# Kernel tuning notes

Hardware: AMD Instinct MI355X
Metric: run time of the kernel (lower is better)

## Reference

```python
import jax, jax.numpy as jnp
import numpy as np

DIM = 512
NUM_HEADS = 16
HEAD_DIM = DIM // NUM_HEADS  # 32
SCALE = HEAD_DIM ** -0.5
B_, N = 1024, 49  # num_windows*batch, window_size**2


def setup_inputs() -> dict:
    key = jax.random.key(0)
    ks = jax.random.split(key, 12)
    s = DIM ** -0.5
    return {
        "x": jax.random.normal(ks[0], (B_, N, DIM), jnp.float32),
        "x2": jax.random.normal(ks[1], (B_, N, DIM), jnp.float32),
        "x3": jax.random.normal(ks[2], (B_, N, DIM), jnp.float32),
        # Linear weights stored as [in, out] (y = x @ W + b), same math as torch Linear
        "Wqkv": jax.random.normal(ks[3], (DIM, 3 * DIM), jnp.float32) * s,
        "bqkv": jnp.zeros((3 * DIM,), jnp.float32),
        "Wqkv2": jax.random.normal(ks[4], (DIM, 3 * DIM), jnp.float32) * s,
        "bqkv2": jnp.zeros((3 * DIM,), jnp.float32),
        "Wgw": jax.random.normal(ks[5], (DIM, DIM), jnp.float32) * s,
        "bgw": jnp.zeros((DIM,), jnp.float32),
        "Wproj": jax.random.normal(ks[6], (DIM, DIM), jnp.float32) * s,
        "bproj": jnp.zeros((DIM,), jnp.float32),
        "a": jnp.zeros((1,), jnp.float32),
    }


def reference(x, x2, x3, Wqkv, bqkv, Wqkv2, bqkv2, Wgw, bgw, Wproj, bproj, a):
    B, Nn, C = x.shape
    H, D = NUM_HEADS, HEAD_DIM
    # qkv from x: only k is actually used downstream
    qkv = (x @ Wqkv + bqkv).reshape(B, Nn, 3, H, D)
    k = jnp.transpose(qkv[:, :, 1], (0, 2, 1, 3))  # [B,H,N,D]
    # qkv2 from x3: q1 (gated query) and v1 (value + residual)
    qkv1 = (x3 @ Wqkv2 + bqkv2).reshape(B, Nn, 3, H, D)
    q1 = jnp.transpose(qkv1[:, :, 0], (0, 2, 1, 3))  # [B,H,N,D]
    v1 = jnp.transpose(qkv1[:, :, 2], (0, 2, 1, 3))  # [B,H,N,D]
    # gate from x2
    gw = jnp.transpose((x2 @ Wgw + bgw).reshape(B, Nn, H, D), (0, 2, 1, 3))
    q = q1 * SCALE * gw
    attn = jax.nn.softmax(jnp.einsum("bhnd,bhmd->bhnm", q, k), axis=-1)
    out = jnp.einsum("bhnm,bhmd->bhnd", attn, v1) + v1 * a
    out = jnp.transpose(out, (0, 2, 1, 3)).reshape(B, Nn, C)
    return out @ Wproj + bproj
```

## Files before the change

### kernel.cpp

```cpp
#include <hip/hip_runtime.h>

#define MR 50176
#define DIMC 512
#define NHEADS 16
#define NWIN 49
#define NBATCH 1024
#define ATTN_SCALE 0.17677669529663689f

typedef short bf16x8 __attribute__((ext_vector_type(8)));
typedef float f32x4 __attribute__((ext_vector_type(4)));
typedef unsigned int u32;

__device__ __forceinline__ unsigned short f2bf(float f) {
  union { float f; u32 u; } v; v.f = f;
  u32 u = v.u;
  u += 0x7FFFu + ((u >> 16) & 1u);
  return (unsigned short)(u >> 16);
}
__device__ __forceinline__ float bits_f(u32 u) {
  union { u32 u; float f; } v; v.u = u; return v.f;
}

__device__ __forceinline__ size_t pk_chunk(int r, int c) {
  return (((size_t)(r >> 3) * 8 + (c >> 3)) * 64 +
          ((r & 7) * 8 + ((c & 7) ^ (r & 7)))) << 4;
}

typedef const __attribute__((address_space(1))) u32* gp_t;
typedef __attribute__((address_space(3))) u32* lp_t;
__device__ __forceinline__ void glds16(const void* g, void* l) {
  __builtin_amdgcn_global_load_lds((gp_t)g, (lp_t)l, 16, 0, 0);
}

__global__ __launch_bounds__(256) void conv_pack(const float* __restrict__ X,
                                                 short* __restrict__ Xp) {
  const int tid = blockIdx.x * 256 + threadIdx.x;
  const int li = tid & 63, gl = tid >> 6;
  const int kline = gl & 7, group = gl >> 3;
  const int rr = li >> 3, pp = li & 7;
  const int row = group * 8 + rr;
  const int k = kline * 64 + ((pp ^ rr) << 3);
  const float* src = X + (size_t)row * DIMC + k;
  const float4 a = *(const float4*)src;
  const float4 b = *(const float4*)(src + 4);
  u32 w0 = (u32)f2bf(a.x) | ((u32)f2bf(a.y) << 16);
  u32 w1 = (u32)f2bf(a.z) | ((u32)f2bf(a.w) << 16);
  u32 w2 = (u32)f2bf(b.x) | ((u32)f2bf(b.y) << 16);
  u32 w3 = (u32)f2bf(b.z) | ((u32)f2bf(b.w) << 16);
  ((uint4*)Xp)[tid] = make_uint4(w0, w1, w2, w3);
}

__global__ __launch_bounds__(256) void prep_w_pack(
    const float* __restrict__ Wqkv, const float* __restrict__ Wqkv2,
    const float* __restrict__ Wgw, const float* __restrict__ Wproj,
    short* __restrict__ Wp) {
  const int tid = blockIdx.x * 256 + threadIdx.x;
  const int li = tid & 63, gl = tid >> 6;
  const int kline = gl & 7, group = gl >> 3;
  const int rr = li >> 3, pp = li & 7;
  const int row = group * 8 + rr;
  const int k = kline * 64 + ((pp ^ rr) << 3);
  const int n = row & 511, mat = row >> 9;
  const float* W; int ldw, col;
  if (mat == 0)      { W = Wqkv;  ldw = 1536; col = 512 + n; }
  else if (mat == 1) { W = Wqkv2; ldw = 1536; col = n; }
  else if (mat == 2) { W = Wqkv2; ldw = 1536; col = 1024 + n; }
  else if (mat == 3) { W = Wgw;   ldw = 512;  col = n; }
  else               { W = Wproj; ldw = 512;  col = n; }
  unsigned short h[8];
#pragma unroll
  for (int j = 0; j < 8; ++j) h[j] = f2bf(W[(size_t)(k + j) * ldw + col]);
  u32 w0 = (u32)h[0] | ((u32)h[1] << 16);
  u32 w1 = (u32)h[2] | ((u32)h[3] << 16);
  u32 w2 = (u32)h[4] | ((u32)h[5] << 16);
  u32 w3 = (u32)h[6] | ((u32)h[7] << 16);
  ((uint4*)Wp)[tid] = make_uint4(w0, w1, w2, w3);
}

template <bool OUT_F32>
__global__ __launch_bounds__(256) void gemm_glds(
    const short* __restrict__ Ap, const short* __restrict__ Wp, int wrow0,
    const float* __restrict__ bias0, const float* __restrict__ bias1,
    short* __restrict__ out0, short* __restrict__ out1,
    float* __restrict__ outf, int nsplit) {
  __shared__ short As[128 * 64];
  __shared__ short Bs[128 * 64];

  const int t = threadIdx.x, w = t >> 6, lane = t & 63;
  const int l15 = lane & 15, q = lane >> 4;
  const int wm = w >> 1, wn = w & 1;
  const int bx = blockIdx.x;
  const int row0 = blockIdx.y * 128;
  const int nw0 = wrow0 + bx * 128;
  const int colsel = (bx < nsplit) ? bx : bx - nsplit;
  const float* bias = (bx < nsplit) ? bias0 : bias1;
  short* outb = (bx < nsplit) ? out0 : out1;
  const int col0 = colsel * 128;

  f32x4 acc[4][4];
#pragma unroll
  for (int i = 0; i < 4; ++i)
#pragma unroll
    for (int j = 0; j < 4; ++j) acc[i][j] = {0.f, 0.f, 0.f, 0.f};

  const size_t lb = (size_t)lane * 16;
  const int r7 = l15 & 7, hi8 = l15 >> 3;

  for (int kt = 0; kt < 8; ++kt) {
    __syncthreads();
#pragma unroll
    for (int jj = 0; jj < 4; ++jj) {
      const int rg = w * 4 + jj;
      const char* ga = (const char*)Ap + ((((size_t)(row0 >> 3) + rg) * 8 + kt) << 10);
      glds16(ga + lb, &As[(size_t)rg << 9]);
      const char* gb = (const char*)Wp + ((((size_t)(nw0 >> 3) + rg) * 8 + kt) << 10);
      glds16(gb + lb, &Bs[(size_t)rg << 9]);
    }
    __syncthreads();
#pragma unroll
    for (int s = 0; s < 2; ++s) {
      const int sw = ((s * 4 + q) ^ r7);
      const int pos = (r7 * 8 + sw) * 8;
      bf16x8 af[4], bfr[4];
#pragma unroll
      for (int i = 0; i < 4; ++i)
        af[i] = *(const bf16x8*)&As[((wm * 8 + i * 2 + hi8) << 9) + pos];
#pragma unroll
      for (int j = 0; j < 4; ++j)
        bfr[j] = *(const bf16x8*)&Bs[((wn * 8 + j * 2 + hi8) << 9) + pos];
#pragma unroll
      for (int i = 0; i < 4; ++i)
#pragma unroll
        for (int j = 0; j < 4; ++j)
          acc[i][j] = __builtin_amdgcn_mfma_f32_16x16x32_bf16(af[i], bfr[j],
                                                              acc[i][j], 0, 0, 0);
    }
  }

#pragma unroll
  for (int j = 0; j < 4; ++j) {
    const int C = col0 + wn * 64 + j * 16 + l15;
    const float bv = bias[C];
#pragma unroll
    for (int i = 0; i < 4; ++i) {
#pragma unroll
      for (int r = 0; r < 4; ++r) {
        const int R = row0 + wm * 64 + i * 16 + q * 4 + r;
        const float val = acc[i][j][r] + bv;
        if constexpr (OUT_F32)
          outf[(size_t)R * DIMC + C] = val;
        else
          *(short*)((char*)outb + pk_chunk(R, C >> 3) + ((C & 7) << 1)) =
              (short)f2bf(val);
      }
    }
  }
}

__global__ __launch_bounds__(256) void attn_mfma(
    const short* __restrict__ kbuf, const short* __restrict__ qbuf,
    const short* __restrict__ vbuf, const short* __restrict__ gbuf,
    const float* __restrict__ a_scalar, short* __restrict__ obuf) {
  __shared__ short pls[4][64 * 40];
  __shared__ short vls[4][32 * 72];

  const int t = threadIdx.x;
  const int w = t >> 6, lane = t & 63;
  const int l15 = lane & 15, q = lane >> 4;
  const int wid = blockIdx.x * 4 + w;
  const int b = wid >> 4, h = wid & 15;
  const int row0 = b * NWIN;
  const float aval = a_scalar[0];
  short* P = pls[w];
  short* VT = vls[w];

#pragma unroll
  for (int it = 0; it < 5; ++it) {
    int off = (it * 64 + lane) * 8;
    if (off < 32 * 72) *(uint4*)&VT[off] = make_uint4(0u, 0u, 0u, 0u);
  }

  bf16x8 kf[4];
#pragma unroll
  for (int mj = 0; mj < 4; ++mj) {
    int m = mj * 16 + l15; if (m > 48) m = 48;
    kf[mj] = *(const bf16x8*)((const char*)kbuf + pk_chunk(row0 + m, h * 4 + q));
  }
  bf16x8 qf[4];
#pragma unroll
  for (int mi = 0; mi < 4; ++mi) {
    int n = mi * 16 + l15; if (n > 48) n = 48;
    const size_t off = pk_chunk(row0 + n, h * 4 + q);
    uint4 qa = *(const uint4*)((const char*)qbuf + off);
    uint4 ga = *(const uint4*)((const char*)gbuf + off);
    u32* qa_ = (u32*)&qa;
    u32* ga_ = (u32*)&ga;
    uint4 res; u32* r_ = (u32*)&res;
#pragma unroll
    for (int jj = 0; jj < 4; ++jj) {
      float lo = bits_f(qa_[jj] << 16) * bits_f(ga_[jj] << 16);
      float hi = bits_f(qa_[jj] & 0xffff0000u) * bits_f(ga_[jj] & 0xffff0000u);
      r_[jj] = (u32)f2bf(lo) | ((u32)f2bf(hi) << 16);
    }
    qf[mi] = *(bf16x8*)&res;
  }
#pragma unroll
  for (int it = 0; it < 4; ++it) {
    int chunk = it * 64 + lane;
    if (chunk < 196) {
      int n = chunk >> 2, dcq = chunk & 3;
      uint4 v = *(const uint4*)((const char*)vbuf + pk_chunk(row0 + n, h * 4 + dcq));
      const short* vs = (const short*)&v;
#pragma unroll
      for (int j = 0; j < 8; ++j) VT[(dcq * 8 + j) * 72 + n] = vs[j];
    }
  }

  f32x4 s[4][4];
#pragma unroll
  for (int mi = 0; mi < 4; ++mi)
#pragma unroll
    for (int nj = 0; nj < 4; ++nj) {
      f32x4 z = {0.f, 0.f, 0.f, 0.f};
      s[mi][nj] = __builtin_amdgcn_mfma_f32_16x16x32_bf16(qf[mi], kf[nj], z, 0, 0, 0);
    }

#pragma unroll
  for (int mi = 0; mi < 4; ++mi)
#pragma unroll
    for (int nj = 0; nj < 4; ++nj) {
      const bool valid = (nj * 16 + l15) < NWIN;
#pragma unroll
      for (int r = 0; r < 4; ++r)
        s[mi][nj][r] = valid ? __expf(ATTN_SCALE * s[mi][nj][r]) : 0.f;
    }

  float lsum[4][4];
#pragma unroll
  for (int mi = 0; mi < 4; ++mi)
#pragma unroll
    for (int r = 0; r < 4; ++r) {
      float part = s[mi][0][r] + s[mi][1][r] + s[mi][2][r] + s[mi][3][r];
      part += __shfl_xor(part, 1, 64);
      part += __shfl_xor(part, 2, 64);
      part += __shfl_xor(part, 4, 64);
      part += __shfl_xor(part, 8, 64);
      lsum[mi][r] = part;
    }

  f32x4 o[4][2];
#pragma unroll
  for (int mi = 0; mi < 4; ++mi)
#pragma unroll
    for (int dj = 0; dj < 2; ++dj) o[mi][dj] = {0.f, 0.f, 0.f, 0.f};

#pragma unroll
  for (int c = 0; c < 2; ++c) {
#pragma unroll
    for (int mi = 0; mi < 4; ++mi)
#pragma unroll
      for (int njh = 0; njh < 2; ++njh) {
        const int nj = c * 2 + njh;
        const int m = nj * 16 + l15;
#pragma unroll
        for (int r = 0; r < 4; ++r) {
          const int n = mi * 16 + q * 4 + r;
          float val = s[mi][nj][r];
          if (m == n) val += aval * lsum[mi][r];
          P[n * 40 + njh * 16 + l15] = (short)f2bf(val);
        }
      }
    bf16x8 bfr[2];
#pragma unroll
    for (int dj = 0; dj < 2; ++dj)
      bfr[dj] = *(const bf16x8*)&VT[(dj * 16 + l15) * 72 + c * 32 + q * 8];
#pragma unroll
    for (int mi = 0; mi < 4; ++mi) {
      bf16x8 af = *(const bf16x8*)&P[(mi * 16 + l15) * 40 + q * 8];
#pragma unroll
      for (int dj = 0; dj < 2; ++dj)
        o[mi][dj] = __builtin_amdgcn_mfma_f32_16x16x32_bf16(af, bfr[dj],
                                                            o[mi][dj], 0, 0, 0);
    }
  }

#pragma unroll
  for (int mi = 0; mi < 4; ++mi)
#pragma unroll
    for (int r = 0; r < 4; ++r) {
      const int n = mi * 16 + q * 4 + r;
      if (n < NWIN) {
        const float rl = 1.0f / lsum[mi][r];
#pragma unroll
        for (int dj = 0; dj < 2; ++dj) {
          const int d = dj * 16 + l15;
          *(short*)((char*)obuf + pk_chunk(row0 + n, h * 4 + (d >> 3)) +
                    ((d & 7) << 1)) = (short)f2bf(o[mi][dj][r] * rl);
        }
      }
    }
}

extern "C" void kernel_launch(void* const* d_in, const int* in_sizes, int n_in,
                              void* d_out, int out_size, void* d_ws,
                              size_t ws_size, hipStream_t stream) {
  const float* x     = (const float*)d_in[0];
  const float* x2    = (const float*)d_in[1];
  const float* x3    = (const float*)d_in[2];
  const float* Wqkv  = (const float*)d_in[3];
  const float* bqkv  = (const float*)d_in[4];
  const float* Wqkv2 = (const float*)d_in[5];
  const float* bqkv2 = (const float*)d_in[6];
  const float* Wgw   = (const float*)d_in[7];
  const float* bgw   = (const float*)d_in[8];
  const float* Wproj = (const float*)d_in[9];
  const float* bproj = (const float*)d_in[10];
  const float* a     = (const float*)d_in[11];

  char* ws = (char*)d_ws;
  const size_t WTSZ = (size_t)2560 * DIMC * sizeof(short);
  const size_t BSZ  = (size_t)MR * DIMC * sizeof(short);
  short* wt_all = (short*)ws;
  short* cb   = (short*)(ws + WTSZ);
  short* kbuf = (short*)(ws + WTSZ + BSZ);
  short* qbuf = (short*)(ws + WTSZ + 2 * BSZ);
  short* vbuf = (short*)(ws + WTSZ + 3 * BSZ);
  short* gbuf = (short*)(ws + WTSZ + 4 * BSZ);
  short* obuf = cb;

  prep_w_pack<<<640, 256, 0, stream>>>(Wqkv, Wqkv2, Wgw, Wproj, wt_all);

  const int convg = MR * DIMC / 8 / 256;
  conv_pack<<<convg, 256, 0, stream>>>(x, cb);
  gemm_glds<false><<<dim3(4, MR / 128), 256, 0, stream>>>(
      cb, wt_all, 0, bqkv + 512, bqkv + 512, kbuf, kbuf, nullptr, 4);
  conv_pack<<<convg, 256, 0, stream>>>(x3, cb);
  gemm_glds<false><<<dim3(8, MR / 128), 256, 0, stream>>>(
      cb, wt_all, 512, bqkv2, bqkv2 + 1024, qbuf, vbuf, nullptr, 4);
  conv_pack<<<convg, 256, 0, stream>>>(x2, cb);
  gemm_glds<false><<<dim3(4, MR / 128), 256, 0, stream>>>(
      cb, wt_all, 1536, bgw, bgw, gbuf, gbuf, nullptr, 4);

  attn_mfma<<<(NBATCH * NHEADS) / 4, 256, 0, stream>>>(kbuf, qbuf, vbuf, gbuf,
                                                       a, obuf);

  gemm_glds<true><<<dim3(4, MR / 128), 256, 0, stream>>>(
      cb, wt_all, 2048, bproj, bproj, nullptr, nullptr, (float*)d_out, 4);
}
```

Baseline: 648.2 us.

## Batch input conversions and projection GEMMs into single launches with XCD-aware block mapping

Converts x, x2 and x3 to packed bf16 in one grid and runs the K, Q, V and gate projection GEMMs as a single grouped launch selected by a per-block config table. Block indices are remapped so that blocks sharing the same row tile stay on the same XCD, aiming for better L2 reuse of the A tiles. This removes several launches and pipeline tails but needs more workspace for separate packed inputs. When the workspace is too small it falls back to the sequential path.

Result: faster. 626.3 us (-3.4%).

```diff
diff --git a/kernel.cpp b/kernel.cpp
--- a/kernel.cpp
+++ b/kernel.cpp
@@ -2,9 +2,9 @@
 
 #define MR 50176
 #define DIMC 512
-#define NHEADS 16
 #define NWIN 49
 #define NBATCH 1024
+#define NHEADS 16
 #define ATTN_SCALE 0.17677669529663689f
 
 typedef short bf16x8 __attribute__((ext_vector_type(8)));
@@ -32,8 +32,12 @@
   __builtin_amdgcn_global_load_lds((gp_t)g, (lp_t)l, 16, 0, 0);
 }
 
-__global__ __launch_bounds__(256) void conv_pack(const float* __restrict__ X,
-                                                 short* __restrict__ Xp) {
+__global__ __launch_bounds__(256) void conv_pack3(
+    const float* __restrict__ X0, const float* __restrict__ X1,
+    const float* __restrict__ X2, short* __restrict__ P0,
+    short* __restrict__ P1, short* __restrict__ P2) {
+  const float* X = (blockIdx.y == 0) ? X0 : (blockIdx.y == 1) ? X1 : X2;
+  short* Xp = (blockIdx.y == 0) ? P0 : (blockIdx.y == 1) ? P1 : P2;
   const int tid = blockIdx.x * 256 + threadIdx.x;
   const int li = tid & 63, gl = tid >> 6;
   const int kline = gl & 7, group = gl >> 3;
@@ -77,25 +81,33 @@
   ((uint4*)Wp)[tid] = make_uint4(w0, w1, w2, w3);
 }
 
-template <bool OUT_F32>
+struct GemmCfg {
+  const short* A[4];
+  const float* bias[4];
+  short* out[4];
+  int wrow0[4];
+};
+
+template <int LNX, bool OUT_F32>
 __global__ __launch_bounds__(256) void gemm_glds(
-    const short* __restrict__ Ap, const short* __restrict__ Wp, int wrow0,
-    const float* __restrict__ bias0, const float* __restrict__ bias1,
-    short* __restrict__ out0, short* __restrict__ out1,
-    float* __restrict__ outf, int nsplit) {
+    GemmCfg cfg, const short* __restrict__ Wp, float* __restrict__ outf) {
   __shared__ short As[128 * 64];
   __shared__ short Bs[128 * 64];
 
   const int t = threadIdx.x, w = t >> 6, lane = t & 63;
   const int l15 = lane & 15, q = lane >> 4;
   const int wm = w >> 1, wn = w & 1;
-  const int bx = blockIdx.x;
-  const int row0 = blockIdx.y * 128;
-  const int nw0 = wrow0 + bx * 128;
-  const int colsel = (bx < nsplit) ? bx : bx - nsplit;
-  const float* bias = (bx < nsplit) ? bias0 : bias1;
-  short* outb = (bx < nsplit) ? out0 : out1;
-  const int col0 = colsel * 128;
+  const int id = blockIdx.x;
+  const int xcd = id & 7, slot = id >> 3;
+  const int bx = slot & ((1 << LNX) - 1);
+  const int y = xcd + ((slot >> LNX) << 3);
+  const int row0 = y * 128;
+  const int unit = bx >> 2, sub = bx & 3;
+  const short* Ap = cfg.A[unit];
+  const float* bias = cfg.bias[unit];
+  short* outb = cfg.out[unit];
+  const int nw0 = cfg.wrow0[unit] + sub * 128;
+  const int col0 = sub * 128;
 
   f32x4 acc[4][4];
 #pragma unroll
@@ -321,29 +333,68 @@
   const size_t WTSZ = (size_t)2560 * DIMC * sizeof(short);
   const size_t BSZ  = (size_t)MR * DIMC * sizeof(short);
   short* wt_all = (short*)ws;
-  short* cb   = (short*)(ws + WTSZ);
-  short* kbuf = (short*)(ws + WTSZ + BSZ);
-  short* qbuf = (short*)(ws + WTSZ + 2 * BSZ);
-  short* vbuf = (short*)(ws + WTSZ + 3 * BSZ);
-  short* gbuf = (short*)(ws + WTSZ + 4 * BSZ);
-  short* obuf = cb;
 
   prep_w_pack<<<640, 256, 0, stream>>>(Wqkv, Wqkv2, Wgw, Wproj, wt_all);
 
   const int convg = MR * DIMC / 8 / 256;
-  conv_pack<<<convg, 256, 0, stream>>>(x, cb);
-  gemm_glds<false><<<dim3(4, MR / 128), 256, 0, stream>>>(
-      cb, wt_all, 0, bqkv + 512, bqkv + 512, kbuf, kbuf, nullptr, 4);
-  conv_pack<<<convg, 256, 0, stream>>>(x3, cb);
-  gemm_glds<false><<<dim3(8, MR / 128), 256, 0, stream>>>(
-      cb, wt_all, 512, bqkv2, bqkv2 + 1024, qbuf, vbuf, nullptr, 4);
-  conv_pack<<<convg, 256, 0, stream>>>(x2, cb);
-  gemm_glds<false><<<dim3(4, MR / 128), 256, 0, stream>>>(
-      cb, wt_all, 1536, bgw, bgw, gbuf, gbuf, nullptr, 4);
-
-  attn_mfma<<<(NBATCH * NHEADS) / 4, 256, 0, stream>>>(kbuf, qbuf, vbuf, gbuf,
-                                                       a, obuf);
-
-  gemm_glds<true><<<dim3(4, MR / 128), 256, 0, stream>>>(
-      cb, wt_all, 2048, bproj, bproj, nullptr, nullptr, (float*)d_out, 4);
-}
+
+  if (ws_size >= WTSZ + 7 * BSZ) {
+    short* xp   = (short*)(ws + WTSZ);
+    short* x2p  = (short*)(ws + WTSZ + BSZ);
+    short* x3p  = (short*)(ws + WTSZ + 2 * BSZ);
+    short* kbuf = (short*)(ws + WTSZ + 3 * BSZ);
+    short* qbuf = (short*)(ws + WTSZ + 4 * BSZ);
+    short* vbuf = (short*)(ws + WTSZ + 5 * BSZ);
+    short* gbuf = (short*)(ws + WTSZ + 6 * BSZ);
+    short* obuf = xp;
+
+    conv_pack3<<<dim3(convg, 3), 256, 0, stream>>>(x, x2, x3, xp, x2p, x3p);
+
+    GemmCfg s1;
+    s1.A[0] = xp;  s1.A[1] = x3p; s1.A[2] = x3p; s1.A[3] = x2p;
+    s1.bias[0] = bqkv + 512; s1.bias[1] = bqkv2;
+    s1.bias[2] = bqkv2 + 1024; s1.bias[3] = bgw;
+    s1.out[0] = kbuf; s1.out[1] = qbuf; s1.out[2] = vbuf; s1.out[3] = gbuf;
+    s1.wrow0[0] = 0; s1.wrow0[1] = 512; s1.wrow0[2] = 1024; s1.wrow0[3] = 1536;
+    gemm_glds<4, false><<<16 * 392, 256, 0, stream>>>(s1, wt_all, nullptr);
+
+    attn_mfma<<<(NBATCH * NHEADS) / 4, 256, 0, stream>>>(kbuf, qbuf, vbuf,
+                                                         gbuf, a, obuf);
+
+    GemmCfg pj = {};
+    pj.A[0] = obuf; pj.bias[0] = bproj; pj.out[0] = nullptr; pj.wrow0[0] = 2048;
+    gemm_glds<2, true><<<4 * 392, 256, 0, stream>>>(pj, wt_all, (float*)d_out);
+  } else {
+    short* cb   = (short*)(ws + WTSZ);
+    short* kbuf = (short*)(ws + WTSZ + BSZ);
+    short* qbuf = (short*)(ws + WTSZ + 2 * BSZ);
+    short* vbuf = (short*)(ws + WTSZ + 3 * BSZ);
+    short* gbuf = (short*)(ws + WTSZ + 4 * BSZ);
+    short* obuf = cb;
+
+    conv_pack3<<<dim3(convg, 1), 256, 0, stream>>>(x, x, x, cb, cb, cb);
+    GemmCfg ck = {};
+    ck.A[0] = cb; ck.bias[0] = bqkv + 512; ck.out[0] = kbuf; ck.wrow0[0] = 0;
+    gemm_glds<2, false><<<4 * 392, 256, 0, stream>>>(ck, wt_all, nullptr);
+
+    conv_pack3<<<dim3(convg, 1), 256, 0, stream>>>(x3, x3, x3, cb, cb, cb);
+    GemmCfg cqv = {};
+    cqv.A[0] = cb; cqv.A[1] = cb;
+    cqv.bias[0] = bqkv2; cqv.bias[1] = bqkv2 + 1024;
+    cqv.out[0] = qbuf; cqv.out[1] = vbuf;
+    cqv.wrow0[0] = 512; cqv.wrow0[1] = 1024;
+    gemm_glds<3, false><<<8 * 392, 256, 0, stream>>>(cqv, wt_all, nullptr);
+
+    conv_pack3<<<dim3(convg, 1), 256, 0, stream>>>(x2, x2, x2, cb, cb, cb);
+    GemmCfg cg = {};
+    cg.A[0] = cb; cg.bias[0] = bgw; cg.out[0] = gbuf; cg.wrow0[0] = 1536;
+    gemm_glds<2, false><<<4 * 392, 256, 0, stream>>>(cg, wt_all, nullptr);
+
+    attn_mfma<<<(NBATCH * NHEADS) / 4, 256, 0, stream>>>(kbuf, qbuf, vbuf,
+                                                         gbuf, a, obuf);
+
+    GemmCfg pj = {};
+    pj.A[0] = obuf; pj.bias[0] = bproj; pj.wrow0[0] = 2048;
+    gemm_glds<2, true><<<4 * 392, 256, 0, stream>>>(pj, wt_all, (float*)d_out);
+  }
+}
```
